# Kernel tuning notes

Measured on AMD Instinct MI355X. Metric: run time of the kernel, lower is better.

## Reference

```python
import jax, jax.numpy as jnp
import numpy as np

N = 128                      # reduced state dimension (Q_dim[0])
S = N * (N + 1) // 2         # number of triu pairwise products = 8256
BATCH = 16384                # snapshot columns
_rows, _cols = np.triu_indices(N)
ROWS = jnp.asarray(_rows)    # [S] int32 constants
COLS = jnp.asarray(_cols)


def setup_inputs() -> dict:
    key = jax.random.key(0)
    kx, ka, kb = jax.random.split(key, 3)
    x = jax.random.normal(kx, (N, BATCH), dtype=jnp.float32)
    # learned operators (module inits them to zeros; use small random for a meaningful baseline)
    A = jax.random.normal(ka, (N, N), dtype=jnp.float32) * 0.02
    B = jax.random.normal(kb, (N, S), dtype=jnp.float32) * 0.02
    return {"x": x, "A": A, "B": B}


def reference(x, A, B):
    # quadratic feature expansion: x2[k, :] = x[i_k, :] * x[j_k, :] over triu pairs
    x2 = x[ROWS] * x[COLS]                 # [S, BATCH]
    return A @ x + B @ x2                  # [N, BATCH]
```

## Files before the change

kernel.cpp:

```cpp
#include <hip/hip_runtime.h>


constexpr int N_     = 128;
constexpr int S_     = 8256;
constexpr int BATCH_ = 16384;
constexpr int KTOT   = 8384;
constexpr int NKT    = 131;
constexpr int LD     = 136;
constexpr size_t WT_BYTES = (size_t)KTOT * 128 * 2;

typedef __attribute__((ext_vector_type(8))) short short8;
typedef __attribute__((ext_vector_type(4))) float f32x4;
typedef __attribute__((ext_vector_type(2))) float f32x2;

__device__ __forceinline__ float bf2f(ushort h) {
    unsigned u = (unsigned)h << 16;
    float f;
    __builtin_memcpy(&f, &u, 4);
    return f;
}
__device__ __forceinline__ ushort f2bf(float f) {
    unsigned u;
    __builtin_memcpy(&u, &f, 4);
    u = (u + 0x7FFFu + ((u >> 16) & 1u)) >> 16;
    return (ushort)u;
}
__device__ __forceinline__ uint fbits(float f) {
    uint u; __builtin_memcpy(&u, &f, 4); return u;
}

__device__ __forceinline__ uint nice_octet(int o) {
    float f = sqrtf(9.0f + 16.0f * (float)o);
    int jb = (int)((3.0f + f) * 0.125f);
    while (jb * (4 * jb - 3) > o) --jb;
    while ((jb + 1) * (4 * jb + 1) <= o) ++jb;
    const int i = o - jb * (4 * jb - 3);
    return (uint)i | ((uint)(jb << 3) << 8);
}

__device__ __forceinline__ uint rag_pair(int c) {
    const int blk = c / 28, rem = c - blk * 28;
    int r, tb;
    if      (rem >= 27) { r = 7; tb = 27; }
    else if (rem >= 25) { r = 6; tb = 25; }
    else if (rem >= 22) { r = 5; tb = 22; }
    else if (rem >= 18) { r = 4; tb = 18; }
    else if (rem >= 13) { r = 3; tb = 13; }
    else if (rem >= 7)  { r = 2; tb = 7;  }
    else                { r = 1; tb = 0;  }
    const int i = blk * 8 + r;
    const int j = i + (rem - tb);
    return (uint)i | ((uint)j << 8);
}

__device__ __forceinline__ float w_value(const float* __restrict__ A,
                                         const float* __restrict__ B,
                                         int m, int k) {
    if (k < 128) return A[m * 128 + k];
    uint p;
    if (k < 7936) {
        p = nice_octet((k - 128) >> 3);
        p += (uint)(k & 7) << 8;
    } else {
        p = rag_pair(k - 7936);
    }
    const int i = (int)(p & 0xFFu), j = (int)(p >> 8);
    const int s = i * (257 - i) / 2 + (j - i);
    return B[(size_t)m * S_ + s];
}

__global__ void prep(const float* __restrict__ A, const float* __restrict__ B,
                     ushort* __restrict__ wt, float* __restrict__ out) {
    const int b = blockIdx.x;
    if (b < 2048) {
        ((float4*)out)[b * 256 + threadIdx.x] = make_float4(0.f, 0.f, 0.f, 0.f);
        return;
    }
    const int e  = (b - 2048) * 256 + threadIdx.x;
    const int kt = e >> 13;
    const int r  = e & 8191;
    const int kk = r >> 12;
    const int wmm = (r >> 11) & 1;
    const int mt = (r >> 9) & 3;
    const int lane = (r >> 3) & 63;
    const int el = r & 7;
    const int m  = wmm * 64 + mt * 16 + (lane & 15);
    const int k  = kt * 64 + kk * 32 + (lane >> 4) * 8 + el;
    wt[e] = f2bf(w_value(A, B, m, k));
}

__device__ __forceinline__ void load_af(short8 af[8], const ushort* __restrict__ wt,
                                        int kt, int wm, int lane) {
    const ushort* ab = wt + ((size_t)kt << 13) + (wm << 11) + (lane << 3);
    #pragma unroll
    for (int kk = 0; kk < 2; ++kk)
        #pragma unroll
        for (int mt = 0; mt < 4; ++mt)
            af[kk * 4 + mt] = *(const short8*)(ab + (kk << 12) + (mt << 9));
}

__device__ __forceinline__ void step_nice(f32x4 acc[4][2], const short8 af[8],
                                          uint prc, const ushort* __restrict__ xr0,
                                          const ushort* __restrict__ xr1) {
    const uint i0a = prc & 0xFFu, j0a = (prc >> 8) & 0xFFu;
    const uint i0b = (prc >> 16) & 0xFFu, j0b = prc >> 24;
    const ushort xia0 = xr0[i0a], xia1 = xr1[i0a];
    const ushort xib0 = xr0[i0b], xib1 = xr1[i0b];
    uint wa0[4], wa1[4], wb0[4], wb1[4];
    __builtin_memcpy(wa0, xr0 + j0a, 16);
    __builtin_memcpy(wa1, xr1 + j0a, 16);
    __builtin_memcpy(wb0, xr0 + j0b, 16);
    __builtin_memcpy(wb1, xr1 + j0b, 16);

    short8 bfr[2][2];
    #pragma unroll
    for (int v = 0; v < 4; ++v) {
        const uint*  wsx = (v == 0) ? wa0 : (v == 1) ? wa1 : (v == 2) ? wb0 : wb1;
        const ushort xis = (v == 0) ? xia0 : (v == 1) ? xia1 : (v == 2) ? xib0 : xib1;
        const float xi = bf2f(xis);
        const f32x2 xi2 = {xi, xi};
        uint ow[4];
        #pragma unroll
        for (int p = 0; p < 4; ++p) {
            const uint lo = wsx[p] << 16;
            const uint hi = wsx[p] & 0xFFFF0000u;
            f32x2 a;
            { float fl, fh;
              __builtin_memcpy(&fl, &lo, 4);
              __builtin_memcpy(&fh, &hi, 4);
              a.x = fl; a.y = fh; }
            const f32x2 o = a * xi2;
            ow[p] = __builtin_amdgcn_perm(fbits(o.y), fbits(o.x),
                                          0x07060302u);
        }
        __builtin_memcpy(&bfr[v >> 1][v & 1], ow, 16);
    }
    #pragma unroll
    for (int kk = 0; kk < 2; ++kk)
        #pragma unroll
        for (int mt = 0; mt < 4; ++mt)
            #pragma unroll
            for (int nt = 0; nt < 2; ++nt)
                acc[mt][nt] = __builtin_amdgcn_mfma_f32_16x16x32_bf16(
                    af[kk * 4 + mt], bfr[kk][nt], acc[mt][nt], 0, 0, 0);
}

__global__ __launch_bounds__(512) void gemm_mfma(
    const float*  __restrict__ x,
    const ushort* __restrict__ wt,
    float* __restrict__ out)
{
    __shared__ ushort xt[128 * LD];
    __shared__ uint   ppc[NKT * 4];

    const int t    = threadIdx.x;
    const int b0   = blockIdx.x * 128;
    const int sp   = blockIdx.y;
    const int kt0  = sp * 33;
    const int kt1  = (sp == 3) ? NKT : kt0 + 33;
    const int lane = t & 63;
    const int w    = t >> 6;
    const int wm   = w >> 2, wn = w & 3;
    const int l16  = lane & 15, quad = lane >> 4;

    {
        const int n = t & 127, g = t >> 7;
        #pragma unroll
        for (int c = 0; c < 4; ++c) {
            const int rb = g * 32 + c * 8;
            uint ow[4];
            #pragma unroll
            for (int p = 0; p < 4; ++p) {
                const ushort u0 = f2bf(x[(size_t)(rb + 2 * p) * BATCH_ + b0 + n]);
                const ushort u1 = f2bf(x[(size_t)(rb + 2 * p + 1) * BATCH_ + b0 + n]);
                ow[p] = (uint)u0 | ((uint)u1 << 16);
            }
            __builtin_memcpy(&xt[n * LD + rb], ow, 16);
        }
    }
    for (int idx = t; idx < NKT * 4; idx += 512) {
        const int kt = idx >> 2, q = idx & 3;
        uint v = 0;
        const int k0 = kt * 64 + q * 8;
        if (k0 >= 128 && k0 + 32 < 7936) {
            const uint a = nice_octet((k0 - 128) >> 3);
            const uint b = nice_octet((k0 + 32 - 128) >> 3);
            v = a | (b << 16);
        }
        ppc[idx] = v;
    }
    __syncthreads();

    f32x4 acc[4][2];
    #pragma unroll
    for (int mt = 0; mt < 4; ++mt)
        #pragma unroll
        for (int nt = 0; nt < 2; ++nt)
            acc[mt][nt] = (f32x4){0.f, 0.f, 0.f, 0.f};

    const ushort* xr0 = xt + (wn * 32 + l16) * LD;
    const ushort* xr1 = xr0 + 16 * LD;

    if (sp == 0) {
        for (int kt = 0; kt < 2; ++kt) {
            short8 af[8];
            load_af(af, wt, kt, wm, lane);
            short8 bfr[2][2];
            #pragma unroll
            for (int kk = 0; kk < 2; ++kk) {
                const int off = kt * 64 + kk * 32 + quad * 8;
                bfr[kk][0] = *(const short8*)(xr0 + off);
                bfr[kk][1] = *(const short8*)(xr1 + off);
            }
            #pragma unroll
            for (int kk = 0; kk < 2; ++kk)
                #pragma unroll
                for (int mt = 0; mt < 4; ++mt)
                    #pragma unroll
                    for (int nt = 0; nt < 2; ++nt)
                        acc[mt][nt] = __builtin_amdgcn_mfma_f32_16x16x32_bf16(
                            af[kk * 4 + mt], bfr[kk][nt], acc[mt][nt], 0, 0, 0);
        }
    }

    {
        const int s_ni = (kt0 > 2) ? kt0 : 2;
        const int e_ni = (kt1 < 124) ? kt1 : 124;
        int kt = s_ni;
        if (kt < e_ni) {
            short8 afA[8], afB[8];
            load_af(afA, wt, kt, wm, lane);
            uint prc = ppc[kt * 4 + quad];
            while (true) {
                {
                    const int ktn = (kt + 1 < e_ni) ? kt + 1 : kt;
                    load_af(afB, wt, ktn, wm, lane);
                    const uint prn = ppc[ktn * 4 + quad];
                    step_nice(acc, afA, prc, xr0, xr1);
                    prc = prn; ++kt;
                }
                if (kt >= e_ni) break;
                {
                    const int ktn = (kt + 1 < e_ni) ? kt + 1 : kt;
                    load_af(afA, wt, ktn, wm, lane);
                    const uint prn = ppc[ktn * 4 + quad];
                    step_nice(acc, afB, prc, xr0, xr1);
                    prc = prn; ++kt;
                }
                if (kt >= e_ni) break;
            }
        }
    }

    if (sp == 3) {
        for (int kt = 124; kt < NKT; ++kt) {
            short8 af[8];
            load_af(af, wt, kt, wm, lane);
            short8 bfr[2][2];
            #pragma unroll
            for (int kk = 0; kk < 2; ++kk) {
                const int cb = kt * 64 + kk * 32 + quad * 8 - 7936;
                uint prs[8];
                #pragma unroll
                for (int e = 0; e < 8; ++e) prs[e] = rag_pair(cb + e);
                #pragma unroll
                for (int nt = 0; nt < 2; ++nt) {
                    const ushort* xr = nt ? xr1 : xr0;
                    float prods[8];
                    #pragma unroll
                    for (int e = 0; e < 8; ++e)
                        prods[e] = bf2f(xr[prs[e] & 0xFFu]) * bf2f(xr[prs[e] >> 8]);
                    uint ow[4];
                    #pragma unroll
                    for (int p = 0; p < 4; ++p)
                        ow[p] = __builtin_amdgcn_perm(fbits(prods[2 * p + 1]),
                                                      fbits(prods[2 * p]),
                                                      0x07060302u);
                    __builtin_memcpy(&bfr[kk][nt], ow, 16);
                }
            }
            #pragma unroll
            for (int kk = 0; kk < 2; ++kk)
                #pragma unroll
                for (int mt = 0; mt < 4; ++mt)
                    #pragma unroll
                    for (int nt = 0; nt < 2; ++nt)
                        acc[mt][nt] = __builtin_amdgcn_mfma_f32_16x16x32_bf16(
                            af[kk * 4 + mt], bfr[kk][nt], acc[mt][nt], 0, 0, 0);
        }
    }

    #pragma unroll
    for (int mt = 0; mt < 4; ++mt) {
        #pragma unroll
        for (int nt = 0; nt < 2; ++nt) {
            const int mbase = wm * 64 + mt * 16 + quad * 4;
            const size_t col = (size_t)b0 + wn * 32 + nt * 16 + l16;
            #pragma unroll
            for (int r = 0; r < 4; ++r)
                unsafeAtomicAdd(&out[(size_t)(mbase + r) * BATCH_ + col],
                                acc[mt][nt][r]);
        }
    }
}

extern "C" void kernel_launch(void* const* d_in, const int* in_sizes, int n_in,
                              void* d_out, int out_size, void* d_ws, size_t ws_size,
                              hipStream_t stream) {
    const float* x = (const float*)d_in[0];
    const float* A = (const float*)d_in[1];
    const float* B = (const float*)d_in[2];
    float* out = (float*)d_out;

    ushort* wt = (ushort*)d_ws;

    prep<<<2048 + 4192, 256, 0, stream>>>(A, B, wt, out);
    gemm_mfma<<<dim3(BATCH_ / 128, 4), 512, 0, stream>>>(x, wt, out);
}
```

Before: 133.8 us.

## Halve K-split to two blocks and prefetch next tile's x-row reads

Splits the K dimension across two blocks per batch tile instead of four. This halves the atomic output adds and the per-block x-tile staging, at the cost of fewer blocks in the grid (256 instead of 512). It also splits the quadratic-feature step into a read phase and a compute phase, so the shared-memory reads of x for the next k-tile are issued before the current tile's MFMAs. That is meant to hide LDS latency, at the cost of more live registers.

```diff
diff --git a/kernel.cpp b/kernel.cpp
--- a/kernel.cpp
+++ b/kernel.cpp
@@ -4,10 +4,8 @@
 constexpr int N_     = 128;
 constexpr int S_     = 8256;
 constexpr int BATCH_ = 16384;
-constexpr int KTOT   = 8384;
 constexpr int NKT    = 131;
 constexpr int LD     = 136;
-constexpr size_t WT_BYTES = (size_t)KTOT * 128 * 2;
 
 typedef __attribute__((ext_vector_type(8))) short short8;
 typedef __attribute__((ext_vector_type(4))) float f32x4;
@@ -99,31 +97,40 @@
             af[kk * 4 + mt] = *(const short8*)(ab + (kk << 12) + (mt << 9));
 }
 
-__device__ __forceinline__ void step_nice(f32x4 acc[4][2], const short8 af[8],
-                                          uint prc, const ushort* __restrict__ xr0,
-                                          const ushort* __restrict__ xr1) {
+struct GenRaw {
+    uint w[4][4];
+    uint xi[4];
+};
+
+__device__ __forceinline__ void gen_read(GenRaw& g, uint prc,
+                                         const ushort* __restrict__ xr0,
+                                         const ushort* __restrict__ xr1) {
     const uint i0a = prc & 0xFFu, j0a = (prc >> 8) & 0xFFu;
     const uint i0b = (prc >> 16) & 0xFFu, j0b = prc >> 24;
-    const ushort xia0 = xr0[i0a], xia1 = xr1[i0a];
-    const ushort xib0 = xr0[i0b], xib1 = xr1[i0b];
-    uint wa0[4], wa1[4], wb0[4], wb1[4];
-    __builtin_memcpy(wa0, xr0 + j0a, 16);
-    __builtin_memcpy(wa1, xr1 + j0a, 16);
-    __builtin_memcpy(wb0, xr0 + j0b, 16);
-    __builtin_memcpy(wb1, xr1 + j0b, 16);
-
+    g.xi[0] = xr0[i0a];
+    g.xi[1] = xr1[i0a];
+    g.xi[2] = xr0[i0b];
+    g.xi[3] = xr1[i0b];
+    __builtin_memcpy(g.w[0], xr0 + j0a, 16);
+    __builtin_memcpy(g.w[1], xr1 + j0a, 16);
+    __builtin_memcpy(g.w[2], xr0 + j0b, 16);
+    __builtin_memcpy(g.w[3], xr1 + j0b, 16);
+}
+
+__device__ __forceinline__ void gen_mfma(f32x4 acc[4][2], const short8 af[8],
+                                         const GenRaw& g) {
     short8 bfr[2][2];
     #pragma unroll
     for (int v = 0; v < 4; ++v) {
-        const uint*  wsx = (v == 0) ? wa0 : (v == 1) ? wa1 : (v == 2) ? wb0 : wb1;
-        const ushort xis = (v == 0) ? xia0 : (v == 1) ? xia1 : (v == 2) ? xib0 : xib1;
-        const float xi = bf2f(xis);
-        const f32x2 xi2 = {xi, xi};
+        const uint xb = g.xi[v] << 16;
+        float xf;
+        __builtin_memcpy(&xf, &xb, 4);
+        const f32x2 xi2 = {xf, xf};
         uint ow[4];
         #pragma unroll
         for (int p = 0; p < 4; ++p) {
-            const uint lo = wsx[p] << 16;
-            const uint hi = wsx[p] & 0xFFFF0000u;
+            const uint lo = g.w[v][p] << 16;
+            const uint hi = g.w[v][p] & 0xFFFF0000u;
             f32x2 a;
             { float fl, fh;
               __builtin_memcpy(&fl, &lo, 4);
@@ -156,8 +163,8 @@
     const int t    = threadIdx.x;
     const int b0   = blockIdx.x * 128;
     const int sp   = blockIdx.y;
-    const int kt0  = sp * 33;
-    const int kt1  = (sp == 3) ? NKT : kt0 + 33;
+    const int kt0  = sp ? 66 : 0;
+    const int kt1  = sp ? NKT : 66;
     const int lane = t & 63;
     const int w    = t >> 6;
     const int wm   = w >> 2, wn = w & 3;
@@ -229,30 +236,31 @@
         int kt = s_ni;
         if (kt < e_ni) {
             short8 afA[8], afB[8];
+            GenRaw rawA, rawB;
             load_af(afA, wt, kt, wm, lane);
-            uint prc = ppc[kt * 4 + quad];
+            gen_read(rawA, ppc[kt * 4 + quad], xr0, xr1);
             while (true) {
                 {
                     const int ktn = (kt + 1 < e_ni) ? kt + 1 : kt;
                     load_af(afB, wt, ktn, wm, lane);
-                    const uint prn = ppc[ktn * 4 + quad];
-                    step_nice(acc, afA, prc, xr0, xr1);
-                    prc = prn; ++kt;
+                    gen_read(rawB, ppc[ktn * 4 + quad], xr0, xr1);
+                    gen_mfma(acc, afA, rawA);
+                    ++kt;
                 }
                 if (kt >= e_ni) break;
                 {
                     const int ktn = (kt + 1 < e_ni) ? kt + 1 : kt;
                     load_af(afA, wt, ktn, wm, lane);
-                    const uint prn = ppc[ktn * 4 + quad];
-                    step_nice(acc, afB, prc, xr0, xr1);
-                    prc = prn; ++kt;
+                    gen_read(rawA, ppc[ktn * 4 + quad], xr0, xr1);
+                    gen_mfma(acc, afB, rawB);
+                    ++kt;
                 }
                 if (kt >= e_ni) break;
             }
         }
     }
 
-    if (sp == 3) {
+    if (sp == 1) {
         for (int kt = 124; kt < NKT; ++kt) {
             short8 af[8];
             load_af(af, wt, kt, wm, lane);
@@ -311,9 +319,8 @@
     const float* A = (const float*)d_in[1];
     const float* B = (const float*)d_in[2];
     float* out = (float*)d_out;
-
     ushort* wt = (ushort*)d_ws;
 
     prep<<<2048 + 4192, 256, 0, stream>>>(A, B, wt, out);
-    gemm_mfma<<<dim3(BATCH_ / 128, 4), 512, 0, stream>>>(x, wt, out);
-}
+    gemm_mfma<<<dim3(BATCH_ / 128, 2), 512, 0, stream>>>(x, wt, out);
+}
```

Result: faster. 126.9 us (-5.2%).
